# Performance work log

Hardware: AMD Instinct MI355X
Metric: run time of the kernel (lower is better)

## Reference

```python
import jax, jax.numpy as jnp
from jax import lax
import numpy as np

NUM_EMBEDDINGS = 512
EMBEDDING_DIM = 64
COMMITMENT_COST = 0.25
SPARSITY_LEVEL = 8


def batch_omp(data, dictionary, max_nonzero):
    """Batch-OMP (Rubinstein et al.).
    data: [D, N], dictionary: [D, K] (columns unit-norm). Returns gamma [K, N].
    Runs a fixed max_nonzero greedy steps (the torch tolerance 1e-7 never
    triggers early exit on random data).
    """
    D, N = data.shape
    K = dictionary.shape[1]
    G = dictionary.T @ dictionary                 # [K, K] Gram matrix
    h_bar = (dictionary.T @ data).T               # [N, K] initial correlations
    h = h_bar
    mask = jnp.zeros((N, K), dtype=bool)          # selected-atom indicator
    rows = jnp.arange(N)
    L = jnp.ones((N, 1, 1), dtype=data.dtype)     # incremental Cholesky of G[I,I]
    I = None                                      # [N, k] selected indices
    x = jnp.zeros((N, K), dtype=data.dtype)
    for k in range(1, max_nonzero + 1):
        # greedy atom selection (masking already-chosen atoms)
        idx = jnp.argmax(jnp.abs(h * (~mask).astype(h.dtype)), axis=1)   # [N]
        mask = mask.at[rows, idx].set(True)
        if k > 1:
            g = G[I, idx[:, None]][..., None]                            # [N, k-1, 1]
            w = lax.linalg.triangular_solve(L, g, left_side=True, lower=True)
            w = jnp.swapaxes(w, 1, 2)                                    # [N, 1, k-1]
            w_corner = jnp.sqrt(1.0 - jnp.sum(w * w, axis=2, keepdims=True))
            top = jnp.concatenate([L, jnp.zeros((N, k - 1, 1), L.dtype)], axis=2)
            bot = jnp.concatenate([w, w_corner], axis=2)
            L = jnp.concatenate([top, bot], axis=1)                      # [N, k, k]
            I = jnp.concatenate([I, idx[:, None]], axis=1)
        else:
            I = idx[:, None]
        hb = jnp.take_along_axis(h_bar, I, axis=1)[..., None]            # [N, k, 1]
        # cholesky_solve: L L^T x = hb
        y = lax.linalg.triangular_solve(L, hb, left_side=True, lower=True)
        xs = lax.linalg.triangular_solve(L, y, left_side=True, lower=True,
                                         transpose_a=True)              # [N, k, 1]
        x = jnp.zeros((N, K), data.dtype).at[rows[:, None], I].set(xs[..., 0])
        beta = x @ G                                                     # x is zero off-support
        h = h_bar - beta
    return x.T                                                           # [K, N]


def setup_inputs() -> dict:
    key = jax.random.key(0)
    k1, k2 = jax.random.split(key)
    z_e = jax.random.normal(k1, (32, EMBEDDING_DIM, 32, 32), dtype=jnp.float32)
    dictionary = jax.random.normal(k2, (EMBEDDING_DIM, NUM_EMBEDDINGS), dtype=jnp.float32)
    beta = jnp.array([1.0 - COMMITMENT_COST], dtype=jnp.float32)  # nn.Parameter(1 - commitment_cost)
    return {"z_e": z_e, "dictionary": dictionary, "beta": beta}


def reference(z_e, dictionary, beta):
    # straight-through column normalization (torch does it via .data assignment)
    Dn_val = dictionary / jnp.linalg.norm(dictionary, axis=0)
    Dn = dictionary + lax.stop_gradient(Dn_val - dictionary)
    zp = jnp.transpose(z_e, (0, 2, 3, 1))                 # [B, H, W, C]
    ze_shape = zp.shape
    zf = zp.reshape(EMBEDDING_DIM, -1)                    # view(D, -1): [D, N]
    gamma = lax.stop_gradient(batch_omp(zf, Dn, SPARSITY_LEVEL))   # [K, N]; copied via .data in torch
    recon = Dn @ gamma                                    # [D, N]
    e_latent_loss = jnp.mean((lax.stop_gradient(recon) - zf) ** 2)
    q_loss = jnp.mean((recon - lax.stop_gradient(zf)) ** 2)
    loss = e_latent_loss * COMMITMENT_COST + beta[0] * q_loss
    recon_st = zf + lax.stop_gradient(recon - zf)         # straight-through
    sm = jax.nn.softmax(gamma, axis=0)
    perplexity = jnp.exp(-jnp.mean(jnp.sum(sm * jnp.log(sm + 1e-10), axis=0)))
    recon_out = jnp.transpose(recon_st.reshape(ze_shape), (0, 3, 1, 2))
    return loss, recon_out, lax.stop_gradient(zf), perplexity, gamma
```

## Files before the change

### kernel.cpp

```cpp
#include <hip/hip_runtime.h>
#include <math.h>

#define NCOL 32768
#define KAT  512
#define DIM  64

#define O_LOSS  0
#define O_RECON 1
#define O_ZF    2097153
#define O_PERP  4194305
#define O_GAMMA 4194306

#define WS_DN   0
#define WS_DNT  32768
#define WS_G    65536
#define WS_ACC  327680

__device__ __forceinline__ float wave_max_bcast_f32(float v) {
    int x = __float_as_int(v);
    int t;
    t = __builtin_amdgcn_update_dpp(x, x, 0x111, 0xf, 0xf, false);
    x = __float_as_int(fmaxf(__int_as_float(x), __int_as_float(t)));
    t = __builtin_amdgcn_update_dpp(x, x, 0x112, 0xf, 0xf, false);
    x = __float_as_int(fmaxf(__int_as_float(x), __int_as_float(t)));
    t = __builtin_amdgcn_update_dpp(x, x, 0x114, 0xf, 0xf, false);
    x = __float_as_int(fmaxf(__int_as_float(x), __int_as_float(t)));
    t = __builtin_amdgcn_update_dpp(x, x, 0x118, 0xf, 0xf, false);
    x = __float_as_int(fmaxf(__int_as_float(x), __int_as_float(t)));
    t = __builtin_amdgcn_update_dpp(x, x, 0x142, 0xa, 0xf, false);
    x = __float_as_int(fmaxf(__int_as_float(x), __int_as_float(t)));
    t = __builtin_amdgcn_update_dpp(x, x, 0x143, 0xc, 0xf, false);
    x = __float_as_int(fmaxf(__int_as_float(x), __int_as_float(t)));
    return __int_as_float(__builtin_amdgcn_readlane(x, 63));
}

__device__ __forceinline__ unsigned wave_min_bcast_u32(unsigned v) {
    int x = (int)v;
    int t;
    t = __builtin_amdgcn_update_dpp(x, x, 0x111, 0xf, 0xf, false);
    x = (int)min((unsigned)x, (unsigned)t);
    t = __builtin_amdgcn_update_dpp(x, x, 0x112, 0xf, 0xf, false);
    x = (int)min((unsigned)x, (unsigned)t);
    t = __builtin_amdgcn_update_dpp(x, x, 0x114, 0xf, 0xf, false);
    x = (int)min((unsigned)x, (unsigned)t);
    t = __builtin_amdgcn_update_dpp(x, x, 0x118, 0xf, 0xf, false);
    x = (int)min((unsigned)x, (unsigned)t);
    t = __builtin_amdgcn_update_dpp(x, x, 0x142, 0xa, 0xf, false);
    x = (int)min((unsigned)x, (unsigned)t);
    t = __builtin_amdgcn_update_dpp(x, x, 0x143, 0xc, 0xf, false);
    x = (int)min((unsigned)x, (unsigned)t);
    return (unsigned)__builtin_amdgcn_readlane(x, 63);
}

__global__ void prep_kernel(const float* __restrict__ dict, float* __restrict__ ws) {
    float* Dn  = ws + WS_DN;
    float* DnT = ws + WS_DNT;
    float* acc = ws + WS_ACC;
    int a = threadIdx.x;
    if (a < 2) acc[a] = 0.f;
    float s = 0.f;
    #pragma unroll
    for (int d = 0; d < DIM; ++d) { float v = dict[d*KAT + a]; s += v * v; }
    float nrm = sqrtf(s);
    #pragma unroll
    for (int d = 0; d < DIM; ++d) {
        float v = dict[d*KAT + a] / nrm;
        Dn[d*KAT + a]  = v;
        DnT[a*DIM + d] = v;
    }
}

__global__ void gram_kernel(const float* __restrict__ ws_in, float* __restrict__ ws) {
    const float* Dn = ws_in + WS_DN;
    float* G = ws + WS_G;
    int i = blockIdx.x, j = threadIdx.x;
    float s = 0.f;
    #pragma unroll
    for (int d = 0; d < DIM; ++d)
        s = fmaf(Dn[d*KAT + i], Dn[d*KAT + j], s);
    G[i*KAT + j] = s;
}

__global__ __launch_bounds__(256) void zf_kernel(const float* __restrict__ z_e,
                                                 float* __restrict__ out) {
    __shared__ float tile[64 * 33];
    int s = blockIdx.x;
    int b = s >> 5, h = s & 31;
    int t = threadIdx.x;
    int srcbase = b * 65536 + h * 32;
    #pragma unroll
    for (int i = 0; i < 8; ++i) {
        int e = t + i * 256;
        int c = e >> 5, w = e & 31;
        tile[c * 33 + w] = z_e[srcbase + c * 1024 + w];
    }
    __syncthreads();
    int obase = O_ZF + s * 2048;
    #pragma unroll
    for (int i = 0; i < 8; ++i) {
        int e = t + i * 256;
        out[obase + e] = tile[(e & 63) * 33 + (e >> 6)];
    }
}

__global__ void gzero_kernel(float2* __restrict__ g2) {
    int id = blockIdx.x * 256 + threadIdx.x;
    #pragma unroll
    for (int i = 0; i < 4; ++i)
        g2[id + i * 2097152] = make_float2(0.f, 0.f);
}

__global__ __launch_bounds__(256) void omp_kernel(const float* __restrict__ z_e,
                                                  const float* __restrict__ ws,
                                                  float* __restrict__ out,
                                                  float* __restrict__ wsw) {
    const float* Dn  = ws + WS_DN;
    const float* DnT = ws + WS_DNT;
    const float* G   = ws + WS_G;
    float* acc = wsw + WS_ACC;

    __shared__ float xcols[DIM * 16];
    __shared__ float hbar[16 * KAT];

    const int t = threadIdx.x;
    const int n_base = blockIdx.x * 16;

    #pragma unroll
    for (int i = 0; i < 4; ++i) {
        int e = t + i * 256;
        int d = e >> 4, c = e & 15;
        int L = d * NCOL + n_base + c;
        int src = (L >> 16) * 65536 + (L & 63) * 1024 + (((L >> 11) & 31) << 5) + ((L >> 6) & 31);
        xcols[e] = z_e[src];
    }
    __syncthreads();

    {
        float a0[16], a1[16];
        #pragma unroll
        for (int i = 0; i < 16; ++i) { a0[i] = 0.f; a1[i] = 0.f; }
        const float4* xc4 = (const float4*)xcols;
        for (int d = 0; d < DIM; ++d) {
            float v0 = Dn[d * KAT + t];
            float v1 = Dn[d * KAT + 256 + t];
            #pragma unroll
            for (int q = 0; q < 4; ++q) {
                float4 xv = xc4[d * 4 + q];
                a0[q*4+0] = fmaf(v0, xv.x, a0[q*4+0]);
                a0[q*4+1] = fmaf(v0, xv.y, a0[q*4+1]);
                a0[q*4+2] = fmaf(v0, xv.z, a0[q*4+2]);
                a0[q*4+3] = fmaf(v0, xv.w, a0[q*4+3]);
                a1[q*4+0] = fmaf(v1, xv.x, a1[q*4+0]);
                a1[q*4+1] = fmaf(v1, xv.y, a1[q*4+1]);
                a1[q*4+2] = fmaf(v1, xv.z, a1[q*4+2]);
                a1[q*4+3] = fmaf(v1, xv.w, a1[q*4+3]);
            }
        }
        #pragma unroll
        for (int c = 0; c < 16; ++c) {
            hbar[c * KAT + t]       = a0[c];
            hbar[c * KAT + 256 + t] = a1[c];
        }
    }
    __syncthreads();

    const int wv = t >> 6, lane = t & 63;
    float wv_sq = 0.f, wv_S = 0.f;

    #pragma unroll 1
    for (int cc = 0; cc < 4; ++cc) {
        const int col = wv * 4 + cc;
        const int n = n_base + col;
        const float* hbcol = hbar + col * KAT;

        float h[8];
        #pragma unroll
        for (int r = 0; r < 8; ++r) h[r] = hbcol[(r << 6) + lane];

        unsigned msk = 0;
        float uv[56];
        float Lr[28];
        float invd[8], yv[8], xr[8];
        int Iv[8];

        #pragma unroll
        for (int k = 0; k < 8; ++k) {
            float bv = -1.f; int bi = 0; float hb = 0.f;
            #pragma unroll
            for (int r = 0; r < 8; ++r) {
                float av = ((msk >> r) & 1) ? -1.f : fabsf(h[r]);
                bool gt = av > bv;
                bv = gt ? av : bv;
                bi = gt ? ((r << 6) | lane) : bi;
                hb = gt ? h[r] : hb;
            }
            float maxv = wave_max_bcast_f32(bv);
            unsigned cand = (bv == maxv) ? (unsigned)bi : 0xffffffffu;
            const int idx = (int)wave_min_bcast_u32(cand);
            unsigned long long sm = __ballot((bv == maxv) && (bi == idx) && (hb < 0.f));
            float hwin = (sm != 0ull) ? -maxv : maxv;

            if ((idx & 63) == lane) msk |= 1u << (idx >> 6);
            Iv[k] = idx;

            const float* grow = G + idx * KAT;
            float gk[8];
            if (k < 7) {
                #pragma unroll
                for (int r = 0; r < 8; ++r) gk[r] = grow[(r << 6) + lane];
            }

            float Lk[7];
            if (k == 0) {
                invd[0] = 1.f;
            } else {
                float s2 = 0.f;
                #pragma unroll
                for (int i = 0; i < 7; ++i) if (i < k) {
                    float a = grow[Iv[i]];
                    #pragma unroll
                    for (int j = 0; j < 7; ++j) if (j < i) a = fmaf(-Lr[i*(i-1)/2 + j], Lk[j], a);
                    Lk[i] = a * invd[i];
                    s2 = fmaf(Lk[i], Lk[i], s2);
                }
                #pragma unroll
                for (int j = 0; j < 7; ++j) if (j < k) Lr[k*(k-1)/2 + j] = Lk[j];
                invd[k] = 1.f / sqrtf(1.f - s2);
            }
            yv[k] = hwin * invd[k];

            if (k < 7) {
                #pragma unroll
                for (int r = 0; r < 8; ++r) {
                    float a = gk[r];
                    #pragma unroll
                    for (int j = 0; j < 7; ++j) if (j < k) a = fmaf(-Lk[j], uv[j*8 + r], a);
                    a *= invd[k];
                    uv[k*8 + r] = a;
                    h[r] = fmaf(-yv[k], a, h[r]);
                }
            }
        }

        #pragma unroll
        for (int i = 7; i >= 0; --i) {
            float a = yv[i];
            #pragma unroll
            for (int j = 0; j < 8; ++j) if (j > i) a = fmaf(-Lr[j*(j-1)/2 + i], xr[j], a);
            xr[i] = a * invd[i];
        }

        #pragma unroll
        for (int j = 0; j < 8; ++j)
            if (lane == j) out[O_GAMMA + Iv[j] * NCOL + n] = xr[j];

        float rec = 0.f;
        #pragma unroll
        for (int j = 0; j < 8; ++j)
            rec = fmaf(xr[j], DnT[Iv[j] * DIM + lane], rec);
        int L = lane * NCOL + n;
        int perm = (L >> 16) * 65536 + (L & 63) * 1024 + (((L >> 11) & 31) << 5) + ((L >> 6) & 31);
        out[O_RECON + perm] = rec;

        float xd = xcols[lane * 16 + col];
        float diff = rec - xd;
        float sq = diff * diff;
        #pragma unroll
        for (int off = 32; off; off >>= 1) sq += __shfl_xor(sq, off, 64);
        if (lane == 0) wv_sq += sq;

        {
            float m = 0.f;
            #pragma unroll
            for (int j = 0; j < 8; ++j) m = fmaxf(m, xr[j]);
            float xsel = 0.f;
            #pragma unroll
            for (int j = 0; j < 8; ++j) xsel = (lane == j) ? xr[j] : xsel;
            float e = (lane < 8) ? expf(xsel - m) : 0.f;
            float se = e;
            #pragma unroll
            for (int off = 1; off < 8; off <<= 1) se += __shfl_xor(se, off, 64);
            float e0 = expf(-m);
            float Z = fmaf(504.f, e0, se);
            float invZ = 1.f / Z;
            float p = e * invZ;
            float tq = (lane < 8) ? p * logf(p + 1e-10f) : 0.f;
            #pragma unroll
            for (int off = 1; off < 8; off <<= 1) tq += __shfl_xor(tq, off, 64);
            if (lane == 0) {
                float p0 = e0 * invZ;
                wv_S += tq + 504.f * p0 * logf(p0 + 1e-10f);
            }
        }
    }

    if (lane == 0) {
        atomicAdd(&acc[0], wv_sq);
        atomicAdd(&acc[1], wv_S);
    }
}

__global__ void fin_kernel(const float* __restrict__ ws, const float* __restrict__ beta,
                           float* __restrict__ out) {
    const float* acc = ws + WS_ACC;
    float mse = acc[0] / 2097152.f;
    out[O_LOSS] = mse * 0.25f + beta[0] * mse;
    out[O_PERP] = expf(-acc[1] / 32768.f);
}

extern "C" void kernel_launch(void* const* d_in, const int* in_sizes, int n_in,
                              void* d_out, int out_size, void* d_ws, size_t ws_size,
                              hipStream_t stream) {
    const float* z_e  = (const float*)d_in[0];
    const float* dict = (const float*)d_in[1];
    const float* beta = (const float*)d_in[2];
    float* out = (float*)d_out;
    float* ws  = (float*)d_ws;

    prep_kernel<<<1, 512, 0, stream>>>(dict, ws);
    gram_kernel<<<512, 512, 0, stream>>>(ws, ws);
    zf_kernel<<<1024, 256, 0, stream>>>(z_e, out);
    gzero_kernel<<<8192, 256, 0, stream>>>((float2*)(out + O_GAMMA));
    omp_kernel<<<2048, 256, 0, stream>>>(z_e, ws, out, ws);
    fin_kernel<<<1, 1, 0, stream>>>(ws, beta, out);
}
```

Baseline: 372.3 us.

## Split OMP into h_bar precompute and per-column kernel, fuse init and finalize

Merges dictionary normalization with gamma zeroing into one init kernel and folds the zf transpose into the h_bar pass. Adds a separate hb_kernel that writes h_bar and the transposed inputs to workspace, and launches the OMP stage with one column per wave in 8192 small blocks instead of 4 columns per wave. The intent is better occupancy and latency hiding, since the old blocks held 32KB of LDS and ran serial column loops. The final loss and perplexity are now computed by the last block through an atomic counter, which removes the fin_kernel launch. The cost is roughly 8MB of extra global round-trip for h_bar, and the fast path only runs when the workspace is large enough.

```diff
diff --git a/kernel.cpp b/kernel.cpp
--- a/kernel.cpp
+++ b/kernel.cpp
@@ -15,6 +15,9 @@
 #define WS_DNT  32768
 #define WS_G    65536
 #define WS_ACC  327680
+#define WS_XT   327696
+#define WS_HB   2424848
+#define WS_NEED (19202064ull * 4ull)
 
 __device__ __forceinline__ float wave_max_bcast_f32(float v) {
     int x = __float_as_int(v);
@@ -52,21 +55,157 @@
     return (unsigned)__builtin_amdgcn_readlane(x, 63);
 }
 
-__global__ void prep_kernel(const float* __restrict__ dict, float* __restrict__ ws) {
-    float* Dn  = ws + WS_DN;
-    float* DnT = ws + WS_DNT;
-    float* acc = ws + WS_ACC;
-    int a = threadIdx.x;
-    if (a < 2) acc[a] = 0.f;
-    float s = 0.f;
-    #pragma unroll
-    for (int d = 0; d < DIM; ++d) { float v = dict[d*KAT + a]; s += v * v; }
-    float nrm = sqrtf(s);
-    #pragma unroll
-    for (int d = 0; d < DIM; ++d) {
-        float v = dict[d*KAT + a] / nrm;
-        Dn[d*KAT + a]  = v;
-        DnT[a*DIM + d] = v;
+__device__ __forceinline__ void omp_column(float h[8], const int n, const int lane,
+                                           const float* __restrict__ G,
+                                           const float* __restrict__ DnT,
+                                           float* __restrict__ out,
+                                           float xd, float& wv_sq, float& wv_S) {
+    unsigned msk = 0;
+    float uv[56], Lr[28], invd[8], yv[8], xr[8];
+    int Iv[8];
+
+    #pragma unroll
+    for (int k = 0; k < 8; ++k) {
+        float bv = -1.f; int bi = 0; float hb = 0.f;
+        #pragma unroll
+        for (int r = 0; r < 8; ++r) {
+            float av = ((msk >> r) & 1) ? -1.f : fabsf(h[r]);
+            bool gt = av > bv;
+            bv = gt ? av : bv;
+            bi = gt ? ((r << 6) | lane) : bi;
+            hb = gt ? h[r] : hb;
+        }
+        float maxv = wave_max_bcast_f32(bv);
+        unsigned cand = (bv == maxv) ? (unsigned)bi : 0xffffffffu;
+        const int idx = (int)wave_min_bcast_u32(cand);
+        unsigned long long sm = __ballot((bv == maxv) && (bi == idx) && (hb < 0.f));
+        float hwin = (sm != 0ull) ? -maxv : maxv;
+
+        if ((idx & 63) == lane) msk |= 1u << (idx >> 6);
+        Iv[k] = idx;
+
+        const float* grow = G + idx * KAT;
+        float gk[8];
+        if (k < 7) {
+            #pragma unroll
+            for (int r = 0; r < 8; ++r) gk[r] = grow[(r << 6) + lane];
+        }
+
+        float Lk[7];
+        if (k == 0) {
+            invd[0] = 1.f;
+        } else {
+            float s2 = 0.f;
+            #pragma unroll
+            for (int i = 0; i < 7; ++i) if (i < k) {
+                float a = grow[Iv[i]];
+                #pragma unroll
+                for (int j = 0; j < 7; ++j) if (j < i)
+                    a = fmaf(-Lr[i*(i-1)/2 + j], Lk[j], a);
+                Lk[i] = a * invd[i];
+                s2 = fmaf(Lk[i], Lk[i], s2);
+            }
+            #pragma unroll
+            for (int j = 0; j < 7; ++j) if (j < k) Lr[k*(k-1)/2 + j] = Lk[j];
+            invd[k] = 1.f / sqrtf(1.f - s2);
+        }
+        yv[k] = hwin * invd[k];
+
+        if (k < 7) {
+            #pragma unroll
+            for (int r = 0; r < 8; ++r) {
+                float a = gk[r];
+                #pragma unroll
+                for (int j = 0; j < 7; ++j) if (j < k)
+                    a = fmaf(-Lk[j], uv[j*8 + r], a);
+                a *= invd[k];
+                uv[k*8 + r] = a;
+                h[r] = fmaf(-yv[k], a, h[r]);
+            }
+        }
+    }
+
+    #pragma unroll
+    for (int i = 7; i >= 0; --i) {
+        float a = yv[i];
+        #pragma unroll
+        for (int j = 0; j < 8; ++j) if (j > i)
+            a = fmaf(-Lr[j*(j-1)/2 + i], xr[j], a);
+        xr[i] = a * invd[i];
+    }
+
+    #pragma unroll
+    for (int j = 0; j < 8; ++j)
+        if (lane == j) out[O_GAMMA + Iv[j] * NCOL + n] = xr[j];
+
+    float rec = 0.f;
+    #pragma unroll
+    for (int j = 0; j < 8; ++j)
+        rec = fmaf(xr[j], DnT[Iv[j] * DIM + lane], rec);
+    int Lf = lane * NCOL + n;
+    int perm = (Lf >> 16) * 65536 + (Lf & 63) * 1024 + (((Lf >> 11) & 31) << 5) + ((Lf >> 6) & 31);
+    out[O_RECON + perm] = rec;
+
+    float diff = rec - xd;
+    float sq = diff * diff;
+    #pragma unroll
+    for (int off = 32; off; off >>= 1) sq += __shfl_xor(sq, off, 64);
+    if (lane == 0) wv_sq += sq;
+
+    {
+        float m = 0.f;
+        #pragma unroll
+        for (int j = 0; j < 8; ++j) m = fmaxf(m, xr[j]);
+        float xsel = 0.f;
+        #pragma unroll
+        for (int j = 0; j < 8; ++j) xsel = (lane == j) ? xr[j] : xsel;
+        float e = (lane < 8) ? expf(xsel - m) : 0.f;
+        float se = e;
+        #pragma unroll
+        for (int off = 1; off < 8; off <<= 1) se += __shfl_xor(se, off, 64);
+        float e0 = expf(-m);
+        float Z = fmaf(504.f, e0, se);
+        float invZ = 1.f / Z;
+        float p = e * invZ;
+        float tq = (lane < 8) ? p * logf(p + 1e-10f) : 0.f;
+        #pragma unroll
+        for (int off = 1; off < 8; off <<= 1) tq += __shfl_xor(tq, off, 64);
+        if (lane == 0) {
+            float p0 = e0 * invZ;
+            wv_S += tq + 504.f * p0 * logf(p0 + 1e-10f);
+        }
+    }
+}
+
+__global__ __launch_bounds__(256) void init_kernel(const float* __restrict__ dict,
+                                                   float* __restrict__ ws,
+                                                   float* __restrict__ out) {
+    int id = blockIdx.x * 256 + threadIdx.x;
+    float2* g2 = (float2*)(out + O_GAMMA);
+    #pragma unroll
+    for (int i = 0; i < 4; ++i)
+        g2[id + i * 2097152] = make_float2(0.f, 0.f);
+
+    if (blockIdx.x == 0) {
+        float* Dn  = ws + WS_DN;
+        float* DnT = ws + WS_DNT;
+        float* acc = ws + WS_ACC;
+        int t = threadIdx.x;
+        if (t == 0) { acc[0] = 0.f; acc[1] = 0.f; ((unsigned*)acc)[2] = 0u; }
+        #pragma unroll
+        for (int half = 0; half < 2; ++half) {
+            int a = t + half * 256;
+            float s = 0.f;
+            #pragma unroll
+            for (int d = 0; d < DIM; ++d) { float v = dict[d*KAT + a]; s += v * v; }
+            float nrm = sqrtf(s);
+            #pragma unroll
+            for (int d = 0; d < DIM; ++d) {
+                float v = dict[d*KAT + a] / nrm;
+                Dn[d*KAT + a]  = v;
+                DnT[a*DIM + d] = v;
+            }
+        }
     }
 }
 
@@ -81,39 +220,116 @@
     G[i*KAT + j] = s;
 }
 
-__global__ __launch_bounds__(256) void zf_kernel(const float* __restrict__ z_e,
+__global__ __launch_bounds__(256) void hb_kernel(const float* __restrict__ z_e,
+                                                 const float* __restrict__ ws,
+                                                 float* __restrict__ wsw,
                                                  float* __restrict__ out) {
-    __shared__ float tile[64 * 33];
-    int s = blockIdx.x;
-    int b = s >> 5, h = s & 31;
-    int t = threadIdx.x;
-    int srcbase = b * 65536 + h * 32;
-    #pragma unroll
-    for (int i = 0; i < 8; ++i) {
+    const float* Dn = ws + WS_DN;
+    float* xT  = wsw + WS_XT;
+    float* hbg = wsw + WS_HB;
+
+    __shared__ float xcols[DIM * 16];
+    __shared__ float xclT[16 * 65];
+
+    const int t = threadIdx.x;
+    const int n_base = blockIdx.x * 16;
+
+    #pragma unroll
+    for (int i = 0; i < 4; ++i) {
         int e = t + i * 256;
-        int c = e >> 5, w = e & 31;
-        tile[c * 33 + w] = z_e[srcbase + c * 1024 + w];
+        int d = e >> 4, c = e & 15;
+        int Lf = d * NCOL + n_base + c;
+        int src = (Lf >> 16) * 65536 + (Lf & 63) * 1024 + (((Lf >> 11) & 31) << 5) + ((Lf >> 6) & 31);
+        float v = z_e[src];
+        xcols[e] = v;
+        xclT[c * 65 + d] = v;
+        out[O_ZF + Lf] = v;
     }
     __syncthreads();
-    int obase = O_ZF + s * 2048;
-    #pragma unroll
-    for (int i = 0; i < 8; ++i) {
+
+    #pragma unroll
+    for (int i = 0; i < 4; ++i) {
         int e = t + i * 256;
-        out[obase + e] = tile[(e & 63) * 33 + (e >> 6)];
-    }
-}
-
-__global__ void gzero_kernel(float2* __restrict__ g2) {
-    int id = blockIdx.x * 256 + threadIdx.x;
-    #pragma unroll
-    for (int i = 0; i < 4; ++i)
-        g2[id + i * 2097152] = make_float2(0.f, 0.f);
-}
-
-__global__ __launch_bounds__(256) void omp_kernel(const float* __restrict__ z_e,
-                                                  const float* __restrict__ ws,
+        int c = e >> 6, d = e & 63;
+        xT[(n_base + c) * DIM + d] = xclT[c * 65 + d];
+    }
+
+    float a0[16], a1[16];
+    #pragma unroll
+    for (int i = 0; i < 16; ++i) { a0[i] = 0.f; a1[i] = 0.f; }
+    const float4* xc4 = (const float4*)xcols;
+    for (int d = 0; d < DIM; ++d) {
+        float v0 = Dn[d * KAT + t];
+        float v1 = Dn[d * KAT + 256 + t];
+        #pragma unroll
+        for (int q = 0; q < 4; ++q) {
+            float4 xv = xc4[d * 4 + q];
+            a0[q*4+0] = fmaf(v0, xv.x, a0[q*4+0]);
+            a0[q*4+1] = fmaf(v0, xv.y, a0[q*4+1]);
+            a0[q*4+2] = fmaf(v0, xv.z, a0[q*4+2]);
+            a0[q*4+3] = fmaf(v0, xv.w, a0[q*4+3]);
+            a1[q*4+0] = fmaf(v1, xv.x, a1[q*4+0]);
+            a1[q*4+1] = fmaf(v1, xv.y, a1[q*4+1]);
+            a1[q*4+2] = fmaf(v1, xv.z, a1[q*4+2]);
+            a1[q*4+3] = fmaf(v1, xv.w, a1[q*4+3]);
+        }
+    }
+    #pragma unroll
+    for (int c = 0; c < 16; ++c) {
+        hbg[(n_base + c) * KAT + t]       = a0[c];
+        hbg[(n_base + c) * KAT + 256 + t] = a1[c];
+    }
+}
+
+__global__ __launch_bounds__(256) void omp_kernel(const float* __restrict__ ws,
+                                                  const float* __restrict__ wsr,
                                                   float* __restrict__ out,
+                                                  const float* __restrict__ beta,
                                                   float* __restrict__ wsw) {
+    const float* DnT = ws + WS_DNT;
+    const float* G   = ws + WS_G;
+    const float* xT  = wsr + WS_XT;
+    const float* hbg = wsr + WS_HB;
+    float* acc = wsw + WS_ACC;
+
+    __shared__ float red[8];
+
+    const int t = threadIdx.x;
+    const int wv = t >> 6, lane = t & 63;
+    const int n = blockIdx.x * 4 + wv;
+
+    float h[8];
+    const float* hb = hbg + n * KAT;
+    #pragma unroll
+    for (int r = 0; r < 8; ++r) h[r] = hb[(r << 6) + lane];
+    float xd = xT[n * DIM + lane];
+
+    float wv_sq = 0.f, wv_S = 0.f;
+    omp_column(h, n, lane, G, DnT, out, xd, wv_sq, wv_S);
+
+    if (lane == 0) { red[wv] = wv_sq; red[4 + wv] = wv_S; }
+    __syncthreads();
+    if (t == 0) {
+        atomicAdd(&acc[0], red[0] + red[1] + red[2] + red[3]);
+        atomicAdd(&acc[1], red[4] + red[5] + red[6] + red[7]);
+        __threadfence();
+        unsigned old = atomicAdd((unsigned*)acc + 2, 1u);
+        if (old == gridDim.x - 1) {
+            __threadfence();
+            float s0 = atomicAdd(&acc[0], 0.f);
+            float s1 = atomicAdd(&acc[1], 0.f);
+            float mse = s0 / 2097152.f;
+            out[O_LOSS] = mse * 0.25f + beta[0] * mse;
+            out[O_PERP] = expf(-s1 / 32768.f);
+        }
+    }
+}
+
+__global__ __launch_bounds__(256) void omp_fused_kernel(const float* __restrict__ z_e,
+                                                        const float* __restrict__ ws,
+                                                        float* __restrict__ out,
+                                                        const float* __restrict__ beta,
+                                                        float* __restrict__ wsw) {
     const float* Dn  = ws + WS_DN;
     const float* DnT = ws + WS_DNT;
     const float* G   = ws + WS_G;
@@ -129,9 +345,11 @@
     for (int i = 0; i < 4; ++i) {
         int e = t + i * 256;
         int d = e >> 4, c = e & 15;
-        int L = d * NCOL + n_base + c;
-        int src = (L >> 16) * 65536 + (L & 63) * 1024 + (((L >> 11) & 31) << 5) + ((L >> 6) & 31);
-        xcols[e] = z_e[src];
+        int Lf = d * NCOL + n_base + c;
+        int src = (Lf >> 16) * 65536 + (Lf & 63) * 1024 + (((Lf >> 11) & 31) << 5) + ((Lf >> 6) & 31);
+        float v = z_e[src];
+        xcols[e] = v;
+        out[O_ZF + Lf] = v;
     }
     __syncthreads();
 
@@ -171,141 +389,30 @@
     for (int cc = 0; cc < 4; ++cc) {
         const int col = wv * 4 + cc;
         const int n = n_base + col;
-        const float* hbcol = hbar + col * KAT;
-
         float h[8];
         #pragma unroll
-        for (int r = 0; r < 8; ++r) h[r] = hbcol[(r << 6) + lane];
-
-        unsigned msk = 0;
-        float uv[56];
-        float Lr[28];
-        float invd[8], yv[8], xr[8];
-        int Iv[8];
-
-        #pragma unroll
-        for (int k = 0; k < 8; ++k) {
-            float bv = -1.f; int bi = 0; float hb = 0.f;
-            #pragma unroll
-            for (int r = 0; r < 8; ++r) {
-                float av = ((msk >> r) & 1) ? -1.f : fabsf(h[r]);
-                bool gt = av > bv;
-                bv = gt ? av : bv;
-                bi = gt ? ((r << 6) | lane) : bi;
-                hb = gt ? h[r] : hb;
-            }
-            float maxv = wave_max_bcast_f32(bv);
-            unsigned cand = (bv == maxv) ? (unsigned)bi : 0xffffffffu;
-            const int idx = (int)wave_min_bcast_u32(cand);
-            unsigned long long sm = __ballot((bv == maxv) && (bi == idx) && (hb < 0.f));
-            float hwin = (sm != 0ull) ? -maxv : maxv;
-
-            if ((idx & 63) == lane) msk |= 1u << (idx >> 6);
-            Iv[k] = idx;
-
-            const float* grow = G + idx * KAT;
-            float gk[8];
-            if (k < 7) {
-                #pragma unroll
-                for (int r = 0; r < 8; ++r) gk[r] = grow[(r << 6) + lane];
-            }
-
-            float Lk[7];
-            if (k == 0) {
-                invd[0] = 1.f;
-            } else {
-                float s2 = 0.f;
-                #pragma unroll
-                for (int i = 0; i < 7; ++i) if (i < k) {
-                    float a = grow[Iv[i]];
-                    #pragma unroll
-                    for (int j = 0; j < 7; ++j) if (j < i) a = fmaf(-Lr[i*(i-1)/2 + j], Lk[j], a);
-                    Lk[i] = a * invd[i];
-                    s2 = fmaf(Lk[i], Lk[i], s2);
-                }
-                #pragma unroll
-                for (int j = 0; j < 7; ++j) if (j < k) Lr[k*(k-1)/2 + j] = Lk[j];
-                invd[k] = 1.f / sqrtf(1.f - s2);
-            }
-            yv[k] = hwin * invd[k];
-
-            if (k < 7) {
-                #pragma unroll
-                for (int r = 0; r < 8; ++r) {
-                    float a = gk[r];
-                    #pragma unroll
-                    for (int j = 0; j < 7; ++j) if (j < k) a = fmaf(-Lk[j], uv[j*8 + r], a);
-                    a *= invd[k];
-                    uv[k*8 + r] = a;
-                    h[r] = fmaf(-yv[k], a, h[r]);
-                }
-            }
-        }
-
-        #pragma unroll
-        for (int i = 7; i >= 0; --i) {
-            float a = yv[i];
-            #pragma unroll
-            for (int j = 0; j < 8; ++j) if (j > i) a = fmaf(-Lr[j*(j-1)/2 + i], xr[j], a);
-            xr[i] = a * invd[i];
-        }
-
-        #pragma unroll
-        for (int j = 0; j < 8; ++j)
-            if (lane == j) out[O_GAMMA + Iv[j] * NCOL + n] = xr[j];
-
-        float rec = 0.f;
-        #pragma unroll
-        for (int j = 0; j < 8; ++j)
-            rec = fmaf(xr[j], DnT[Iv[j] * DIM + lane], rec);
-        int L = lane * NCOL + n;
-        int perm = (L >> 16) * 65536 + (L & 63) * 1024 + (((L >> 11) & 31) << 5) + ((L >> 6) & 31);
-        out[O_RECON + perm] = rec;
-
+        for (int r = 0; r < 8; ++r) h[r] = hbar[col * KAT + (r << 6) + lane];
         float xd = xcols[lane * 16 + col];
-        float diff = rec - xd;
-        float sq = diff * diff;
-        #pragma unroll
-        for (int off = 32; off; off >>= 1) sq += __shfl_xor(sq, off, 64);
-        if (lane == 0) wv_sq += sq;
-
-        {
-            float m = 0.f;
-            #pragma unroll
-            for (int j = 0; j < 8; ++j) m = fmaxf(m, xr[j]);
-            float xsel = 0.f;
-            #pragma unroll
-            for (int j = 0; j < 8; ++j) xsel = (lane == j) ? xr[j] : xsel;
-            float e = (lane < 8) ? expf(xsel - m) : 0.f;
-            float se = e;
-            #pragma unroll
-            for (int off = 1; off < 8; off <<= 1) se += __shfl_xor(se, off, 64);
-            float e0 = expf(-m);
-            float Z = fmaf(504.f, e0, se);
-            float invZ = 1.f / Z;
-            float p = e * invZ;
-            float tq = (lane < 8) ? p * logf(p + 1e-10f) : 0.f;
-            #pragma unroll
-            for (int off = 1; off < 8; off <<= 1) tq += __shfl_xor(tq, off, 64);
-            if (lane == 0) {
-                float p0 = e0 * invZ;
-                wv_S += tq + 504.f * p0 * logf(p0 + 1e-10f);
-            }
-        }
+        omp_column(h, n, lane, G, DnT, out, xd, wv_sq, wv_S);
     }
 
     if (lane == 0) {
         atomicAdd(&acc[0], wv_sq);
         atomicAdd(&acc[1], wv_S);
     }
-}
-
-__global__ void fin_kernel(const float* __restrict__ ws, const float* __restrict__ beta,
-                           float* __restrict__ out) {
-    const float* acc = ws + WS_ACC;
-    float mse = acc[0] / 2097152.f;
-    out[O_LOSS] = mse * 0.25f + beta[0] * mse;
-    out[O_PERP] = expf(-acc[1] / 32768.f);
+    __threadfence();
+    __syncthreads();
+    if (t == 0) {
+        unsigned old = atomicAdd((unsigned*)acc + 2, 1u);
+        if (old == gridDim.x - 1) {
+            __threadfence();
+            float s0 = atomicAdd(&acc[0], 0.f);
+            float s1 = atomicAdd(&acc[1], 0.f);
+            float mse = s0 / 2097152.f;
+            out[O_LOSS] = mse * 0.25f + beta[0] * mse;
+            out[O_PERP] = expf(-s1 / 32768.f);
+        }
+    }
 }
 
 extern "C" void kernel_launch(void* const* d_in, const int* in_sizes, int n_in,
@@ -317,10 +424,12 @@
     float* out = (float*)d_out;
     float* ws  = (float*)d_ws;
 
-    prep_kernel<<<1, 512, 0, stream>>>(dict, ws);
+    init_kernel<<<8192, 256, 0, stream>>>(dict, ws, out);
     gram_kernel<<<512, 512, 0, stream>>>(ws, ws);
-    zf_kernel<<<1024, 256, 0, stream>>>(z_e, out);
-    gzero_kernel<<<8192, 256, 0, stream>>>((float2*)(out + O_GAMMA));
-    omp_kernel<<<2048, 256, 0, stream>>>(z_e, ws, out, ws);
-    fin_kernel<<<1, 1, 0, stream>>>(ws, beta, out);
-}
+    if (ws_size >= WS_NEED) {
+        hb_kernel<<<2048, 256, 0, stream>>>(z_e, ws, ws, out);
+        omp_kernel<<<8192, 256, 0, stream>>>(ws, ws, out, beta, ws);
+    } else {
+        omp_fused_kernel<<<2048, 256, 0, stream>>>(z_e, ws, out, beta, ws);
+    }
+}
```

Result: slower. 521.5 us (+40.1%).

## Fuse prep, zero-fill, zf copy and finalize into fewer kernels

Applied to the files above, without the earlier changes.

Folds dictionary normalization and the gamma zero-fill into one init kernel. The z_e-to-zf copy now happens inside the OMP kernel's column load, and a last-block-done atomic counter replaces the separate finalize kernel. Reconstruction values are staged in swizzled LDS and written out per block instead of per-wave scattered stores. Shuffle reductions become DPP reductions and fast exp/log intrinsics are used. This cuts launches and redundant global traffic, at the cost of a grid-wide atomic completion protocol and slightly lower transcendental accuracy.

```diff
diff --git a/kernel.cpp b/kernel.cpp
--- a/kernel.cpp
+++ b/kernel.cpp
@@ -52,21 +52,69 @@
     return (unsigned)__builtin_amdgcn_readlane(x, 63);
 }
 
-__global__ void prep_kernel(const float* __restrict__ dict, float* __restrict__ ws) {
-    float* Dn  = ws + WS_DN;
-    float* DnT = ws + WS_DNT;
-    float* acc = ws + WS_ACC;
-    int a = threadIdx.x;
-    if (a < 2) acc[a] = 0.f;
-    float s = 0.f;
+__device__ __forceinline__ float wave_sum_f32(float v) {
+    float x = v;
+    int t;
+    t = __builtin_amdgcn_update_dpp(0, __float_as_int(x), 0x111, 0xf, 0xf, true);
+    x += __int_as_float(t);
+    t = __builtin_amdgcn_update_dpp(0, __float_as_int(x), 0x112, 0xf, 0xf, true);
+    x += __int_as_float(t);
+    t = __builtin_amdgcn_update_dpp(0, __float_as_int(x), 0x114, 0xf, 0xf, true);
+    x += __int_as_float(t);
+    t = __builtin_amdgcn_update_dpp(0, __float_as_int(x), 0x118, 0xf, 0xf, true);
+    x += __int_as_float(t);
+    t = __builtin_amdgcn_update_dpp(0, __float_as_int(x), 0x142, 0xa, 0xf, false);
+    x += __int_as_float(t);
+    t = __builtin_amdgcn_update_dpp(0, __float_as_int(x), 0x143, 0xc, 0xf, false);
+    x += __int_as_float(t);
+    return __int_as_float(__builtin_amdgcn_readlane(__float_as_int(x), 63));
+}
+
+__device__ __forceinline__ float sum8_f32(float v) {
+    float x = v;
+    int t;
+    t = __builtin_amdgcn_update_dpp(0, __float_as_int(x), 0xB1, 0xf, 0xf, false);
+    x += __int_as_float(t);
+    t = __builtin_amdgcn_update_dpp(0, __float_as_int(x), 0x4E, 0xf, 0xf, false);
+    x += __int_as_float(t);
+    t = __builtin_amdgcn_update_dpp(0, __float_as_int(x), 0x141, 0xf, 0xf, false);
+    x += __int_as_float(t);
+    return x;
+}
+
+__global__ __launch_bounds__(256) void init_kernel(const float* __restrict__ dict,
+                                                   float* __restrict__ ws,
+                                                   float* __restrict__ out) {
+    int id = blockIdx.x * 256 + threadIdx.x;
+    float4* g4 = (float4*)(out + 4194304);
+    float4 z = make_float4(0.f, 0.f, 0.f, 0.f);
     #pragma unroll
-    for (int d = 0; d < DIM; ++d) { float v = dict[d*KAT + a]; s += v * v; }
-    float nrm = sqrtf(s);
-    #pragma unroll
-    for (int d = 0; d < DIM; ++d) {
-        float v = dict[d*KAT + a] / nrm;
-        Dn[d*KAT + a]  = v;
-        DnT[a*DIM + d] = v;
+    for (int i = 0; i < 4; ++i)
+        g4[id + i * 1048576] = z;
+
+    if (blockIdx.x == 0) {
+        int t = threadIdx.x;
+        if (t == 0) {
+            out[20971520] = 0.f; out[20971521] = 0.f;
+        }
+        float* Dn  = ws + WS_DN;
+        float* DnT = ws + WS_DNT;
+        float* acc = ws + WS_ACC;
+        if (t == 0) { acc[0] = 0.f; acc[1] = 0.f; ((unsigned*)acc)[2] = 0u; }
+        #pragma unroll
+        for (int half = 0; half < 2; ++half) {
+            int a = t + half * 256;
+            float s = 0.f;
+            #pragma unroll
+            for (int d = 0; d < DIM; ++d) { float v = dict[d*KAT + a]; s += v * v; }
+            float nrm = sqrtf(s);
+            #pragma unroll
+            for (int d = 0; d < DIM; ++d) {
+                float v = dict[d*KAT + a] / nrm;
+                Dn[d*KAT + a]  = v;
+                DnT[a*DIM + d] = v;
+            }
+        }
     }
 }
 
@@ -81,38 +129,10 @@
     G[i*KAT + j] = s;
 }
 
-__global__ __launch_bounds__(256) void zf_kernel(const float* __restrict__ z_e,
-                                                 float* __restrict__ out) {
-    __shared__ float tile[64 * 33];
-    int s = blockIdx.x;
-    int b = s >> 5, h = s & 31;
-    int t = threadIdx.x;
-    int srcbase = b * 65536 + h * 32;
-    #pragma unroll
-    for (int i = 0; i < 8; ++i) {
-        int e = t + i * 256;
-        int c = e >> 5, w = e & 31;
-        tile[c * 33 + w] = z_e[srcbase + c * 1024 + w];
-    }
-    __syncthreads();
-    int obase = O_ZF + s * 2048;
-    #pragma unroll
-    for (int i = 0; i < 8; ++i) {
-        int e = t + i * 256;
-        out[obase + e] = tile[(e & 63) * 33 + (e >> 6)];
-    }
-}
-
-__global__ void gzero_kernel(float2* __restrict__ g2) {
-    int id = blockIdx.x * 256 + threadIdx.x;
-    #pragma unroll
-    for (int i = 0; i < 4; ++i)
-        g2[id + i * 2097152] = make_float2(0.f, 0.f);
-}
-
 __global__ __launch_bounds__(256) void omp_kernel(const float* __restrict__ z_e,
                                                   const float* __restrict__ ws,
                                                   float* __restrict__ out,
+                                                  const float* __restrict__ beta,
                                                   float* __restrict__ wsw) {
     const float* Dn  = ws + WS_DN;
     const float* DnT = ws + WS_DNT;
@@ -121,6 +141,7 @@
 
     __shared__ float xcols[DIM * 16];
     __shared__ float hbar[16 * KAT];
+    __shared__ float lds_rec[DIM * 16];
 
     const int t = threadIdx.x;
     const int n_base = blockIdx.x * 16;
@@ -129,9 +150,11 @@
     for (int i = 0; i < 4; ++i) {
         int e = t + i * 256;
         int d = e >> 4, c = e & 15;
-        int L = d * NCOL + n_base + c;
-        int src = (L >> 16) * 65536 + (L & 63) * 1024 + (((L >> 11) & 31) << 5) + ((L >> 6) & 31);
-        xcols[e] = z_e[src];
+        int Lf = d * NCOL + n_base + c;
+        int src = (Lf >> 16) * 65536 + (Lf & 63) * 1024 + (((Lf >> 11) & 31) << 5) + ((Lf >> 6) & 31);
+        float v = z_e[src];
+        xcols[e] = v;
+        out[O_ZF + Lf] = v;
     }
     __syncthreads();
 
@@ -196,7 +219,8 @@
             }
             float maxv = wave_max_bcast_f32(bv);
             unsigned cand = (bv == maxv) ? (unsigned)bi : 0xffffffffu;
-            const int idx = (int)wave_min_bcast_u32(cand);
+            const int idx = __builtin_amdgcn_readfirstlane(
+                                (int)wave_min_bcast_u32(cand));
             unsigned long long sm = __ballot((bv == maxv) && (bi == idx) && (hb < 0.f));
             float hwin = (sm != 0ull) ? -maxv : maxv;
 
@@ -219,7 +243,8 @@
                 for (int i = 0; i < 7; ++i) if (i < k) {
                     float a = grow[Iv[i]];
                     #pragma unroll
-                    for (int j = 0; j < 7; ++j) if (j < i) a = fmaf(-Lr[i*(i-1)/2 + j], Lk[j], a);
+                    for (int j = 0; j < 7; ++j) if (j < i)
+                        a = fmaf(-Lr[i*(i-1)/2 + j], Lk[j], a);
                     Lk[i] = a * invd[i];
                     s2 = fmaf(Lk[i], Lk[i], s2);
                 }
@@ -234,7 +259,8 @@
                 for (int r = 0; r < 8; ++r) {
                     float a = gk[r];
                     #pragma unroll
-                    for (int j = 0; j < 7; ++j) if (j < k) a = fmaf(-Lk[j], uv[j*8 + r], a);
+                    for (int j = 0; j < 7; ++j) if (j < k)
+                        a = fmaf(-Lk[j], uv[j*8 + r], a);
                     a *= invd[k];
                     uv[k*8 + r] = a;
                     h[r] = fmaf(-yv[k], a, h[r]);
@@ -246,27 +272,31 @@
         for (int i = 7; i >= 0; --i) {
             float a = yv[i];
             #pragma unroll
-            for (int j = 0; j < 8; ++j) if (j > i) a = fmaf(-Lr[j*(j-1)/2 + i], xr[j], a);
+            for (int j = 0; j < 8; ++j) if (j > i)
+                a = fmaf(-Lr[j*(j-1)/2 + i], xr[j], a);
             xr[i] = a * invd[i];
         }
 
-        #pragma unroll
-        for (int j = 0; j < 8; ++j)
-            if (lane == j) out[O_GAMMA + Iv[j] * NCOL + n] = xr[j];
+        {
+            float gv = xr[0]; int ai = Iv[0];
+            #pragma unroll
+            for (int j = 1; j < 8; ++j) {
+                bool m = (lane == j);
+                gv = m ? xr[j] : gv;
+                ai = m ? Iv[j] : ai;
+            }
+            if (lane < 8) out[O_GAMMA + ai * NCOL + n] = gv;
+        }
 
         float rec = 0.f;
         #pragma unroll
         for (int j = 0; j < 8; ++j)
             rec = fmaf(xr[j], DnT[Iv[j] * DIM + lane], rec);
-        int L = lane * NCOL + n;
-        int perm = (L >> 16) * 65536 + (L & 63) * 1024 + (((L >> 11) & 31) << 5) + ((L >> 6) & 31);
-        out[O_RECON + perm] = rec;
+        lds_rec[lane * 16 + (col ^ (lane & 15))] = rec;
 
         float xd = xcols[lane * 16 + col];
         float diff = rec - xd;
-        float sq = diff * diff;
-        #pragma unroll
-        for (int off = 32; off; off >>= 1) sq += __shfl_xor(sq, off, 64);
+        float sq = wave_sum_f32(diff * diff);
         if (lane == 0) wv_sq += sq;
 
         {
@@ -276,36 +306,49 @@
             float xsel = 0.f;
             #pragma unroll
             for (int j = 0; j < 8; ++j) xsel = (lane == j) ? xr[j] : xsel;
-            float e = (lane < 8) ? expf(xsel - m) : 0.f;
-            float se = e;
-            #pragma unroll
-            for (int off = 1; off < 8; off <<= 1) se += __shfl_xor(se, off, 64);
-            float e0 = expf(-m);
+            float e = (lane < 8) ? __expf(xsel - m) : 0.f;
+            float se = sum8_f32(e);
+            float e0 = __expf(-m);
             float Z = fmaf(504.f, e0, se);
             float invZ = 1.f / Z;
             float p = e * invZ;
-            float tq = (lane < 8) ? p * logf(p + 1e-10f) : 0.f;
-            #pragma unroll
-            for (int off = 1; off < 8; off <<= 1) tq += __shfl_xor(tq, off, 64);
+            float tq = (lane < 8) ? p * __logf(p + 1e-10f) : 0.f;
+            tq = sum8_f32(tq);
             if (lane == 0) {
                 float p0 = e0 * invZ;
-                wv_S += tq + 504.f * p0 * logf(p0 + 1e-10f);
-            }
-        }
+                wv_S += tq + 504.f * p0 * __logf(p0 + 1e-10f);
+            }
+        }
+    }
+
+    __syncthreads();
+    #pragma unroll
+    for (int i = 0; i < 4; ++i) {
+        int e = t + i * 256;
+        int d = e >> 4, c = e & 15;
+        float rec = lds_rec[d * 16 + (c ^ (d & 15))];
+        int Lf = d * NCOL + n_base + c;
+        int perm = (Lf >> 16) * 65536 + (Lf & 63) * 1024 + (((Lf >> 11) & 31) << 5) + ((Lf >> 6) & 31);
+        out[O_RECON + perm] = rec;
     }
 
     if (lane == 0) {
         atomicAdd(&acc[0], wv_sq);
         atomicAdd(&acc[1], wv_S);
     }
-}
-
-__global__ void fin_kernel(const float* __restrict__ ws, const float* __restrict__ beta,
-                           float* __restrict__ out) {
-    const float* acc = ws + WS_ACC;
-    float mse = acc[0] / 2097152.f;
-    out[O_LOSS] = mse * 0.25f + beta[0] * mse;
-    out[O_PERP] = expf(-acc[1] / 32768.f);
+    __threadfence();
+    __syncthreads();
+    if (t == 0) {
+        unsigned old = atomicAdd((unsigned*)acc + 2, 1u);
+        if (old == gridDim.x - 1) {
+            __threadfence();
+            float s0 = atomicAdd(&acc[0], 0.f);
+            float s1 = atomicAdd(&acc[1], 0.f);
+            float mse = s0 / 2097152.f;
+            out[O_LOSS] = mse * 0.25f + beta[0] * mse;
+            out[O_PERP] = __expf(-s1 / 32768.f);
+        }
+    }
 }
 
 extern "C" void kernel_launch(void* const* d_in, const int* in_sizes, int n_in,
@@ -317,10 +360,7 @@
     float* out = (float*)d_out;
     float* ws  = (float*)d_ws;
 
-    prep_kernel<<<1, 512, 0, stream>>>(dict, ws);
+    init_kernel<<<4096, 256, 0, stream>>>(dict, ws, out);
     gram_kernel<<<512, 512, 0, stream>>>(ws, ws);
-    zf_kernel<<<1024, 256, 0, stream>>>(z_e, out);
-    gzero_kernel<<<8192, 256, 0, stream>>>((float2*)(out + O_GAMMA));
-    omp_kernel<<<2048, 256, 0, stream>>>(z_e, ws, out, ws);
-    fin_kernel<<<1, 1, 0, stream>>>(ws, beta, out);
-}
+    omp_kernel<<<2048, 256, 0, stream>>>(z_e, ws, out, beta, ws);
+}
```

Result: slower. 519.2 us (+39.5%).
